# Optimization experiments

Hardware: AMD Instinct MI355X
Metric: run time of the kernel (lower is better)

Reference implementation:

```python
import jax, jax.numpy as jnp
import numpy as np

B, K, LQ, LR, H = 32, 8, 128, 256, 512  # H = hidden_dim*2
L = LQ + K * LR


def setup_inputs() -> dict:
    key = jax.random.key(0)
    ks = jax.random.split(key, 10)
    w = 0.02
    return {
        "h_q": jax.random.normal(ks[0], (B, LQ, H), jnp.float32),
        "q_mask": jnp.ones((B, LQ), jnp.float32),
        "h_r": jax.random.normal(ks[1], (B, K, LR, H), jnp.float32),
        "r_mask": jnp.ones((B, K, LR), jnp.float32),
        "s_t": jax.random.normal(ks[2], (B, H), jnp.float32),
        "qr_cov": jnp.zeros((B, L), jnp.float32),
        # Linear weights stored torch-style [out, in]
        "U_w": jax.random.normal(ks[3], (H, H), jnp.float32) * w,
        "Wc_w": jax.random.normal(ks[4], (H, 1), jnp.float32) * w,
        "Ws_w": jax.random.normal(ks[5], (H, H), jnp.float32) * w,
        "Wqr_w": jax.random.normal(ks[6], (H, H), jnp.float32) * w,
        "Wqr_b": jax.random.normal(ks[7], (H,), jnp.float32) * w,
        "Vr_w": jax.random.normal(ks[8], (1, H), jnp.float32) * w,
    }


def reference(h_q, q_mask, h_r, r_mask, s_t, qr_cov,
              U_w, Wc_w, Ws_w, Wqr_w, Wqr_b, Vr_w):
    b, l_q, h = h_q.shape
    _, k, l_r, _ = h_r.shape

    _h_q = jnp.broadcast_to(h_q[:, None], (b, k, l_q, h)).reshape(b * k, l_q, h)
    _h_r = h_r.reshape(b * k, l_r, h)
    _q_mask = jnp.broadcast_to(q_mask[:, None], (b, k, l_q)).reshape(b * k, l_q)
    _r_mask = r_mask.reshape(b * k, l_r)

    # bilinear co-attention scores: tanh((hq @ U^T) @ hr^T)  [b*k, l_q, l_r]
    hqU = jnp.einsum('bqi,oi->bqo', _h_q, U_w)
    U = jnp.tanh(jnp.einsum('bqo,bro->bqr', hqU, _h_r))

    alpha_q = jax.nn.softmax(jnp.max(U, axis=2), axis=-1)  # [b*k, l_q]
    alpha_r = jax.nn.softmax(jnp.max(U, axis=1), axis=-1)  # [b*k, l_r]

    pai_q = ((alpha_q * _q_mask)[..., None] * _h_q).reshape(b, k, l_q, h).mean(axis=1)
    pai_r = ((alpha_r * _r_mask)[..., None] * _h_r).reshape(b, k * l_r, h)
    qr = jnp.concatenate([pai_q, pai_r], axis=1)  # [b, L, h]

    dec_fea = (jnp.einsum('bi,oi->bo', s_t, Ws_w)[:, None, :]
               + jnp.einsum('bli,oi->blo', qr, Wqr_w) + Wqr_b
               + qr_cov[:, :, None] * Wc_w[:, 0])  # coverage feature

    logits = jnp.einsum('blo,o->bl', jnp.tanh(dec_fea), Vr_w[0])  # [b, L]
    mask = jnp.concatenate([q_mask, r_mask.reshape(b, k * l_r)], axis=1)
    a = jax.nn.softmax(logits, axis=1) * mask
    a = a / jnp.sum(a, axis=1, keepdims=True)

    c_t = jnp.einsum('bl,blh->bh', a, qr)
    new_cov = qr_cov + a
    return (c_t, a, new_cov)
```

## Files before the change

### kernel.cpp

```cpp
#include <hip/hip_runtime.h>
#include <stdint.h>

#define B  32
#define KK 8
#define LQ 128
#define LR 256
#define H  512
#define LL 2176
#define STRIDE 40

typedef short s16x8 __attribute__((ext_vector_type(8)));
typedef float f32x4 __attribute__((ext_vector_type(4)));

__device__ __forceinline__ unsigned short f2bf(float f) {
    unsigned int u = __float_as_uint(f);
    unsigned int r = (u + 0x7FFFu + ((u >> 16) & 1u)) >> 16;
    return (unsigned short)r;
}
__device__ __forceinline__ float bf2f(unsigned short h) {
    return __uint_as_float(((unsigned int)h) << 16);
}

__global__ __launch_bounds__(128) void k0_convert(
    const float* __restrict__ h_q, const float* __restrict__ h_r,
    const float* __restrict__ U_w, const float* __restrict__ Wqr_w,
    unsigned short* __restrict__ Xb, unsigned short* __restrict__ Uwb,
    unsigned short* __restrict__ Wqrb) {
    int blk = blockIdx.x;
    const float* src; unsigned short* dst;
    if (blk < B * LL) {
        int b = blk / LL, l = blk % LL;
        src = (l < LQ) ? (h_q + (size_t)(b * LQ + l) * H)
                       : (h_r + (size_t)(b * (KK * LR) + (l - LQ)) * H);
        dst = Xb + (size_t)blk * H;
    } else if (blk < B * LL + H) {
        int i = blk - B * LL;
        src = U_w + (size_t)i * H; dst = Uwb + (size_t)i * H;
    } else {
        int i = blk - B * LL - H;
        src = Wqr_w + (size_t)i * H; dst = Wqrb + (size_t)i * H;
    }
    int t = threadIdx.x;
    float4 v = *(const float4*)(src + t * 4);
    ushort4 o;
    o.x = f2bf(v.x); o.y = f2bf(v.y); o.z = f2bf(v.z); o.w = f2bf(v.w);
    *(ushort4*)(dst + t * 4) = o;
}

__global__ __launch_bounds__(256) void k1_gemm_hqU(
    const unsigned short* __restrict__ Xb, const unsigned short* __restrict__ Uwb,
    unsigned short* __restrict__ hqU) {
    __shared__ __align__(16) unsigned short As[64 * STRIDE];
    __shared__ __align__(16) unsigned short Bs[64 * STRIDE];
    int tid = threadIdx.x;
    int wave = tid >> 6, lane = tid & 63;
    int quad = lane >> 4, l16 = lane & 15;
    int wr = wave >> 1, wc = wave & 1;
    int m0 = blockIdx.x * 64, n0 = blockIdx.y * 64;

    f32x4 acc[2][2] = {};
    int srow = tid >> 2, sk8 = tid & 3;
    int am = m0 + srow;
    size_t arow = (size_t)(am >> 7) * LL + (am & 127);
    for (int k0 = 0; k0 < H; k0 += 32) {
        *(uint4*)&As[srow * STRIDE + sk8 * 8] =
            *(const uint4*)(Xb + arow * H + k0 + sk8 * 8);
        *(uint4*)&Bs[srow * STRIDE + sk8 * 8] =
            *(const uint4*)(Uwb + (size_t)(n0 + srow) * H + k0 + sk8 * 8);
        __syncthreads();
        s16x8 af[2], bfr[2];
#pragma unroll
        for (int mi = 0; mi < 2; ++mi)
            af[mi] = *(const s16x8*)&As[(wr * 32 + mi * 16 + l16) * STRIDE + quad * 8];
#pragma unroll
        for (int ni = 0; ni < 2; ++ni)
            bfr[ni] = *(const s16x8*)&Bs[(wc * 32 + ni * 16 + l16) * STRIDE + quad * 8];
#pragma unroll
        for (int mi = 0; mi < 2; ++mi)
#pragma unroll
            for (int ni = 0; ni < 2; ++ni)
                acc[mi][ni] = __builtin_amdgcn_mfma_f32_16x16x32_bf16(
                    af[mi], bfr[ni], acc[mi][ni], 0, 0, 0);
        __syncthreads();
    }
#pragma unroll
    for (int mi = 0; mi < 2; ++mi)
#pragma unroll
        for (int ni = 0; ni < 2; ++ni)
#pragma unroll
            for (int i = 0; i < 4; ++i) {
                int row = m0 + wr * 32 + mi * 16 + quad * 4 + i;
                int col = n0 + wc * 32 + ni * 16 + l16;
                hqU[(size_t)row * H + col] = f2bf(acc[mi][ni][i]);
            }
}

__global__ __launch_bounds__(256) void k2_scores(
    const unsigned short* __restrict__ hqU, const unsigned short* __restrict__ Xb,
    float* __restrict__ maxq_part, float* __restrict__ maxr_part) {
    __shared__ __align__(16) unsigned short As[64 * STRIDE];
    __shared__ __align__(16) unsigned short Bs[128 * STRIDE];
    __shared__ float redA[64 * 2];
    __shared__ float redB[128 * 2];
    int idx = blockIdx.x;
    int rt = idx & 1, qt = (idx >> 1) & 1, k = (idx >> 2) & 7, b = idx >> 5;
    int tid = threadIdx.x;
    int wave = tid >> 6, lane = tid & 63;
    int quad = lane >> 4, l16 = lane & 15;
    int wr = wave >> 1, wc = wave & 1;

    size_t aBase = (size_t)(b * LQ + qt * 64) * H;
    size_t bBase = (size_t)(b * LL + LQ + k * LR + rt * 128) * H;

    f32x4 acc[2][4] = {};
    int srow = tid >> 2, sk8 = tid & 3;
    for (int k0 = 0; k0 < H; k0 += 32) {
        *(uint4*)&As[srow * STRIDE + sk8 * 8] =
            *(const uint4*)(hqU + aBase + (size_t)srow * H + k0 + sk8 * 8);
        for (int c = tid; c < 512; c += 256) {
            int br = c >> 2, bk8 = c & 3;
            *(uint4*)&Bs[br * STRIDE + bk8 * 8] =
                *(const uint4*)(Xb + bBase + (size_t)br * H + k0 + bk8 * 8);
        }
        __syncthreads();
        s16x8 af[2], bfr[4];
#pragma unroll
        for (int mi = 0; mi < 2; ++mi)
            af[mi] = *(const s16x8*)&As[(wr * 32 + mi * 16 + l16) * STRIDE + quad * 8];
#pragma unroll
        for (int ni = 0; ni < 4; ++ni)
            bfr[ni] = *(const s16x8*)&Bs[(wc * 64 + ni * 16 + l16) * STRIDE + quad * 8];
#pragma unroll
        for (int mi = 0; mi < 2; ++mi)
#pragma unroll
            for (int ni = 0; ni < 4; ++ni)
                acc[mi][ni] = __builtin_amdgcn_mfma_f32_16x16x32_bf16(
                    af[mi], bfr[ni], acc[mi][ni], 0, 0, 0);
        __syncthreads();
    }
#pragma unroll
    for (int mi = 0; mi < 2; ++mi)
#pragma unroll
        for (int i = 0; i < 4; ++i) {
            float v = acc[mi][0][i];
            v = fmaxf(v, acc[mi][1][i]);
            v = fmaxf(v, acc[mi][2][i]);
            v = fmaxf(v, acc[mi][3][i]);
            for (int s = 1; s < 16; s <<= 1) v = fmaxf(v, __shfl_xor(v, s));
            if (l16 == 0) redA[(wr * 32 + mi * 16 + quad * 4 + i) * 2 + wc] = v;
        }
#pragma unroll
    for (int ni = 0; ni < 4; ++ni) {
        float v = acc[0][ni][0];
#pragma unroll
        for (int mi = 0; mi < 2; ++mi)
#pragma unroll
            for (int i = 0; i < 4; ++i) v = fmaxf(v, acc[mi][ni][i]);
        for (int s = 16; s < 64; s <<= 1) v = fmaxf(v, __shfl_xor(v, s));
        if (quad == 0) redB[(wc * 64 + ni * 16 + l16) * 2 + wr] = v;
    }
    __syncthreads();
    size_t base = (size_t)(b * KK + k);
    if (tid < 64) {
        float v = fmaxf(redA[tid * 2 + 0], redA[tid * 2 + 1]);
        maxq_part[(base * 2 + rt) * 128 + qt * 64 + tid] = v;
    }
    if (tid < 128) {
        float v = fmaxf(redB[tid * 2 + 0], redB[tid * 2 + 1]);
        maxr_part[(base * 2 + qt) * 256 + rt * 128 + tid] = v;
    }
}

__global__ __launch_bounds__(256) void k3a_alphas(
    const float* __restrict__ maxq_part, const float* __restrict__ maxr_part,
    const float* __restrict__ r_mask, float* __restrict__ alpha_q,
    float* __restrict__ wbuf) {
    int b = blockIdx.x >> 3, k = blockIdx.x & 7;
    int t = threadIdx.x;
    __shared__ float red[256];
    size_t base = (size_t)(b * KK + k);
    float vq = -1e30f;
    if (t < 128)
        vq = tanhf(fmaxf(maxq_part[(base * 2 + 0) * 128 + t],
                         maxq_part[(base * 2 + 1) * 128 + t]));
    red[t] = vq; __syncthreads();
    for (int s = 128; s > 0; s >>= 1) { if (t < s) red[t] = fmaxf(red[t], red[t + s]); __syncthreads(); }
    float mxq = red[0]; __syncthreads();
    float eq = (t < 128) ? expf(vq - mxq) : 0.f;
    red[t] = eq; __syncthreads();
    for (int s = 128; s > 0; s >>= 1) { if (t < s) red[t] += red[t + s]; __syncthreads(); }
    float invq = 1.f / red[0]; __syncthreads();
    if (t < 128) alpha_q[base * 128 + t] = eq * invq;
    float vr = tanhf(fmaxf(maxr_part[(base * 2 + 0) * 256 + t],
                           maxr_part[(base * 2 + 1) * 256 + t]));
    red[t] = vr; __syncthreads();
    for (int s = 128; s > 0; s >>= 1) { if (t < s) red[t] = fmaxf(red[t], red[t + s]); __syncthreads(); }
    float mxr = red[0]; __syncthreads();
    float er = expf(vr - mxr);
    red[t] = er; __syncthreads();
    for (int s = 128; s > 0; s >>= 1) { if (t < s) red[t] += red[t + s]; __syncthreads(); }
    float invr = 1.f / red[0];
    wbuf[b * LL + LQ + k * LR + t] = r_mask[base * LR + t] * er * invr;
}

__global__ __launch_bounds__(256) void k3b_wq_sws(
    const float* __restrict__ alpha_q, const float* __restrict__ q_mask,
    const float* __restrict__ s_t, const float* __restrict__ Ws_w,
    float* __restrict__ wbuf, float* __restrict__ logits,
    float* __restrict__ sWs, float* __restrict__ out_ct) {
    int b = blockIdx.x, t = threadIdx.x;
    for (int l = t; l < LL; l += 256) logits[b * LL + l] = 0.f;
    if (t < 128) {
        float s = 0.f;
#pragma unroll
        for (int k = 0; k < KK; ++k) s += alpha_q[(size_t)(b * KK + k) * 128 + t];
        wbuf[b * LL + t] = q_mask[b * LQ + t] * s * 0.125f;
    }
    out_ct[b * H + t] = 0.f;
    out_ct[b * H + 256 + t] = 0.f;
    __shared__ __align__(16) float sl[H];
    for (int i = t; i < H; i += 256) sl[i] = s_t[b * H + i];
    __syncthreads();
    const float4* sl4 = (const float4*)sl;
    for (int o = t; o < H; o += 256) {
        const float4* wr4 = (const float4*)(Ws_w + (size_t)o * H);
        float a = 0.f;
        for (int i = 0; i < H / 4; ++i) {
            float4 x = sl4[i], y = wr4[i];
            a += x.x * y.x + x.y * y.y + x.z * y.z + x.w * y.w;
        }
        sWs[b * H + o] = a;
    }
}

__global__ __launch_bounds__(256) void k4_gemm_logits(
    const unsigned short* __restrict__ Xb, const unsigned short* __restrict__ Wqrb,
    const float* __restrict__ sWs, const float* __restrict__ Wqr_b,
    const float* __restrict__ Wc_w, const float* __restrict__ Vr_w,
    const float* __restrict__ wbuf, const float* __restrict__ qr_cov,
    float* __restrict__ logits) {
    __shared__ __align__(16) unsigned short As[128 * STRIDE];
    __shared__ __align__(16) unsigned short Bs[128 * STRIDE];
    __shared__ float wrow[128], covrow[128], sWsl[128], biasl[128], wcl[128], vrl[128];
    int tid = threadIdx.x;
    int wave = tid >> 6, lane = tid & 63;
    int quad = lane >> 4, l16 = lane & 15;
    int wr = wave >> 1, wc = wave & 1;
    size_t m0 = (size_t)blockIdx.x * 128;
    int n0 = blockIdx.y * 128;
    int b = (int)(m0 / LL);
    int l0 = (int)(m0 % LL);

    f32x4 acc[4][4] = {};
    for (int k0 = 0; k0 < H; k0 += 32) {
        for (int c = tid; c < 512; c += 256) {
            int r = c >> 2, k8 = c & 3;
            *(uint4*)&As[r * STRIDE + k8 * 8] =
                *(const uint4*)(Xb + (m0 + r) * H + k0 + k8 * 8);
            *(uint4*)&Bs[r * STRIDE + k8 * 8] =
                *(const uint4*)(Wqrb + (size_t)(n0 + r) * H + k0 + k8 * 8);
        }
        __syncthreads();
        s16x8 af[4], bfr[4];
#pragma unroll
        for (int mi = 0; mi < 4; ++mi)
            af[mi] = *(const s16x8*)&As[(wr * 64 + mi * 16 + l16) * STRIDE + quad * 8];
#pragma unroll
        for (int ni = 0; ni < 4; ++ni)
            bfr[ni] = *(const s16x8*)&Bs[(wc * 64 + ni * 16 + l16) * STRIDE + quad * 8];
#pragma unroll
        for (int mi = 0; mi < 4; ++mi)
#pragma unroll
            for (int ni = 0; ni < 4; ++ni)
                acc[mi][ni] = __builtin_amdgcn_mfma_f32_16x16x32_bf16(
                    af[mi], bfr[ni], acc[mi][ni], 0, 0, 0);
        __syncthreads();
    }
    if (tid < 128) {
        wrow[tid]   = wbuf[b * LL + l0 + tid];
        covrow[tid] = qr_cov[b * LL + l0 + tid];
        sWsl[tid]   = sWs[b * H + n0 + tid];
        biasl[tid]  = Wqr_b[n0 + tid];
        wcl[tid]    = Wc_w[n0 + tid];
        vrl[tid]    = Vr_w[n0 + tid];
    }
    __syncthreads();
#pragma unroll
    for (int mi = 0; mi < 4; ++mi)
#pragma unroll
        for (int i = 0; i < 4; ++i) {
            int rl = wr * 64 + mi * 16 + quad * 4 + i;
            float wv = wrow[rl], cv = covrow[rl];
            float lsum = 0.f;
#pragma unroll
            for (int ni = 0; ni < 4; ++ni) {
                int ol = wc * 64 + ni * 16 + l16;
                float dec = sWsl[ol] + wv * acc[mi][ni][i] + biasl[ol] + cv * wcl[ol];
                lsum += vrl[ol] * tanhf(dec);
            }
            for (int s = 1; s < 16; s <<= 1) lsum += __shfl_xor(lsum, s);
            if (l16 == 0) atomicAdd(&logits[b * LL + l0 + rl], lsum);
        }
}

__global__ __launch_bounds__(256) void k5a_softmax(
    const float* __restrict__ logits, const float* __restrict__ q_mask,
    const float* __restrict__ r_mask, const float* __restrict__ qr_cov,
    const float* __restrict__ wbuf, float* __restrict__ out,
    float* __restrict__ coef) {
    int b = blockIdx.x, t = threadIdx.x;
    __shared__ float red[256];
    float mx = -1e30f;
    for (int l = t; l < LL; l += 256) mx = fmaxf(mx, logits[b * LL + l]);
    red[t] = mx; __syncthreads();
    for (int s = 128; s > 0; s >>= 1) { if (t < s) red[t] = fmaxf(red[t], red[t + s]); __syncthreads(); }
    mx = red[0]; __syncthreads();
    float sum = 0.f;
    for (int l = t; l < LL; l += 256) {
        float e = expf(logits[b * LL + l] - mx);
        float m = (l < LQ) ? q_mask[b * LQ + l] : r_mask[b * (KK * LR) + l - LQ];
        sum += e * m;
    }
    red[t] = sum; __syncthreads();
    for (int s = 128; s > 0; s >>= 1) { if (t < s) red[t] += red[t + s]; __syncthreads(); }
    float inv = 1.f / red[0];
    float* aout = out + B * H + (size_t)b * LL;
    float* cov  = out + B * H + (size_t)B * LL + (size_t)b * LL;
    for (int l = t; l < LL; l += 256) {
        float e = expf(logits[b * LL + l] - mx);
        float m = (l < LQ) ? q_mask[b * LQ + l] : r_mask[b * (KK * LR) + l - LQ];
        float a = e * m * inv;
        aout[l] = a;
        cov[l] = qr_cov[b * LL + l] + a;
        coef[b * LL + l] = a * wbuf[b * LL + l];
    }
}

__global__ __launch_bounds__(256) void k5b_ct(
    const unsigned short* __restrict__ Xb, const float* __restrict__ coef,
    float* __restrict__ out) {
    int b = blockIdx.x / 17, chunk = blockIdx.x % 17;
    int t = threadIdx.x;
    int l0 = chunk * 128;
    __shared__ float cl[128];
    if (t < 128) cl[t] = coef[b * LL + l0 + t];
    __syncthreads();
    float a0 = 0.f, a1 = 0.f;
    const unsigned short* xp = Xb + ((size_t)b * LL + l0) * H;
    for (int l = 0; l < 128; ++l) {
        float c = cl[l];
        a0 += c * bf2f(xp[(size_t)l * H + t]);
        a1 += c * bf2f(xp[(size_t)l * H + t + 256]);
    }
    atomicAdd(&out[b * H + t], a0);
    atomicAdd(&out[b * H + t + 256], a1);
}

extern "C" void kernel_launch(void* const* d_in, const int* in_sizes, int n_in,
                              void* d_out, int out_size, void* d_ws, size_t ws_size,
                              hipStream_t stream) {
    (void)in_sizes; (void)n_in; (void)out_size; (void)ws_size;
    const float* h_q    = (const float*)d_in[0];
    const float* q_mask = (const float*)d_in[1];
    const float* h_r    = (const float*)d_in[2];
    const float* r_mask = (const float*)d_in[3];
    const float* s_t    = (const float*)d_in[4];
    const float* qr_cov = (const float*)d_in[5];
    const float* U_w    = (const float*)d_in[6];
    const float* Wc_w   = (const float*)d_in[7];
    const float* Ws_w   = (const float*)d_in[8];
    const float* Wqr_w  = (const float*)d_in[9];
    const float* Wqr_b  = (const float*)d_in[10];
    const float* Vr_w   = (const float*)d_in[11];
    float* out = (float*)d_out;

    char* p = (char*)d_ws;
    unsigned short* Xb   = (unsigned short*)p; p += (size_t)B * LL * H * 2;
    unsigned short* Uwb  = (unsigned short*)p; p += (size_t)H * H * 2;
    unsigned short* Wqrb = (unsigned short*)p; p += (size_t)H * H * 2;
    unsigned short* hqU  = (unsigned short*)p; p += (size_t)B * LQ * H * 2;
    float* sWs       = (float*)p; p += (size_t)B * H * 4;
    float* maxq_part = (float*)p; p += (size_t)B * KK * 2 * 128 * 4;
    float* maxr_part = (float*)p; p += (size_t)B * KK * 2 * 256 * 4;
    float* alpha_q   = (float*)p; p += (size_t)B * KK * 128 * 4;
    float* wbuf      = (float*)p; p += (size_t)B * LL * 4;
    float* logits    = (float*)p; p += (size_t)B * LL * 4;
    float* coef      = (float*)p; p += (size_t)B * LL * 4;

    k0_convert<<<B * LL + 2 * H, 128, 0, stream>>>(h_q, h_r, U_w, Wqr_w, Xb, Uwb, Wqrb);
    k1_gemm_hqU<<<dim3((B * LQ) / 64, H / 64), 256, 0, stream>>>(Xb, Uwb, hqU);
    k2_scores<<<B * KK * 4, 256, 0, stream>>>(hqU, Xb, maxq_part, maxr_part);
    k3a_alphas<<<B * KK, 256, 0, stream>>>(maxq_part, maxr_part, r_mask, alpha_q, wbuf);
    k3b_wq_sws<<<B, 256, 0, stream>>>(alpha_q, q_mask, s_t, Ws_w, wbuf, logits, sWs, out);
    k4_gemm_logits<<<dim3((B * LL) / 128, H / 128), 256, 0, stream>>>(
        Xb, Wqrb, sWs, Wqr_b, Wc_w, Vr_w, wbuf, qr_cov, logits);
    k5a_softmax<<<B, 256, 0, stream>>>(logits, q_mask, r_mask, qr_cov, wbuf, out, coef);
    k5b_ct<<<B * (LL / 128), 256, 0, stream>>>(Xb, coef, out);
}
```

Before: 405.0 us.

## Use direct global-to-LDS loads with swizzle, parallelize sWs, vectorize c_t

```diff
diff --git a/kernel.cpp b/kernel.cpp
--- a/kernel.cpp
+++ b/kernel.cpp
@@ -20,13 +20,29 @@
 __device__ __forceinline__ float bf2f(unsigned short h) {
     return __uint_as_float(((unsigned int)h) << 16);
 }
-
+__device__ __forceinline__ void gload16(const unsigned short* g, unsigned short* l) {
+    __builtin_amdgcn_global_load_lds(
+        (const __attribute__((address_space(1))) void*)g,
+        (__attribute__((address_space(3))) void*)l, 16, 0, 0);
+}
+
+#define NCONV (B * LL + 2 * H)
+#define NZERO 168
 __global__ __launch_bounds__(128) void k0_convert(
     const float* __restrict__ h_q, const float* __restrict__ h_r,
     const float* __restrict__ U_w, const float* __restrict__ Wqr_w,
     unsigned short* __restrict__ Xb, unsigned short* __restrict__ Uwb,
-    unsigned short* __restrict__ Wqrb) {
+    unsigned short* __restrict__ Wqrb, float* __restrict__ logits,
+    float* __restrict__ out) {
     int blk = blockIdx.x;
+    int t = threadIdx.x;
+    if (blk >= NCONV) {
+        int base = (blk - NCONV) * 512 + t * 4;
+        float4 z = {0.f, 0.f, 0.f, 0.f};
+        if (base < B * LL) *(float4*)(logits + base) = z;
+        else *(float4*)(out + base - B * LL) = z;
+        return;
+    }
     const float* src; unsigned short* dst;
     if (blk < B * LL) {
         int b = blk / LL, l = blk % LL;
@@ -40,7 +56,6 @@
         int i = blk - B * LL - H;
         src = Wqr_w + (size_t)i * H; dst = Wqrb + (size_t)i * H;
     }
-    int t = threadIdx.x;
     float4 v = *(const float4*)(src + t * 4);
     ushort4 o;
     o.x = f2bf(v.x); o.y = f2bf(v.y); o.z = f2bf(v.z); o.w = f2bf(v.w);
@@ -98,8 +113,8 @@
 __global__ __launch_bounds__(256) void k2_scores(
     const unsigned short* __restrict__ hqU, const unsigned short* __restrict__ Xb,
     float* __restrict__ maxq_part, float* __restrict__ maxr_part) {
-    __shared__ __align__(16) unsigned short As[64 * STRIDE];
-    __shared__ __align__(16) unsigned short Bs[128 * STRIDE];
+    __shared__ __align__(16) unsigned short As[64 * 64];
+    __shared__ __align__(16) unsigned short Bs[128 * 64];
     __shared__ float redA[64 * 2];
     __shared__ float redB[128 * 2];
     int idx = blockIdx.x;
@@ -109,33 +124,55 @@
     int quad = lane >> 4, l16 = lane & 15;
     int wr = wave >> 1, wc = wave & 1;
 
-    size_t aBase = (size_t)(b * LQ + qt * 64) * H;
-    size_t bBase = (size_t)(b * LL + LQ + k * LR + rt * 128) * H;
+    const unsigned short* Ab = hqU + (size_t)(b * LQ + qt * 64) * H;
+    const unsigned short* Bb = Xb + (size_t)(b * LL + LQ + k * LR + rt * 128) * H;
+
+    const unsigned short* ag[2]; unsigned short* la[2];
+    const unsigned short* bg[4]; unsigned short* lb[4];
+#pragma unroll
+    for (int i = 0; i < 2; ++i) {
+        int g = (wave * 2 + i) * 64 + lane;
+        int r = g >> 3, c = g & 7, cs = c ^ (r & 7);
+        ag[i] = Ab + (size_t)r * H + cs * 8;
+        la[i] = As + (wave * 2 + i) * 512;
+    }
+#pragma unroll
+    for (int i = 0; i < 4; ++i) {
+        int g = (wave * 4 + i) * 64 + lane;
+        int r = g >> 3, c = g & 7, cs = c ^ (r & 7);
+        bg[i] = Bb + (size_t)r * H + cs * 8;
+        lb[i] = Bs + (wave * 4 + i) * 512;
+    }
 
     f32x4 acc[2][4] = {};
-    int srow = tid >> 2, sk8 = tid & 3;
-    for (int k0 = 0; k0 < H; k0 += 32) {
-        *(uint4*)&As[srow * STRIDE + sk8 * 8] =
-            *(const uint4*)(hqU + aBase + (size_t)srow * H + k0 + sk8 * 8);
-        for (int c = tid; c < 512; c += 256) {
-            int br = c >> 2, bk8 = c & 3;
-            *(uint4*)&Bs[br * STRIDE + bk8 * 8] =
-                *(const uint4*)(Xb + bBase + (size_t)br * H + k0 + bk8 * 8);
+    for (int k0 = 0; k0 < H; k0 += 64) {
+#pragma unroll
+        for (int i = 0; i < 2; ++i) gload16(ag[i] + k0, la[i]);
+#pragma unroll
+        for (int i = 0; i < 4; ++i) gload16(bg[i] + k0, lb[i]);
+        __syncthreads();
+#pragma unroll
+        for (int kh = 0; kh < 2; ++kh) {
+            s16x8 af[2], bfr[4];
+#pragma unroll
+            for (int mi = 0; mi < 2; ++mi) {
+                int row = wr * 32 + mi * 16 + l16;
+                int ch = (kh * 4 + quad) ^ (row & 7);
+                af[mi] = *(const s16x8*)&As[(row * 8 + ch) * 8];
+            }
+#pragma unroll
+            for (int ni = 0; ni < 4; ++ni) {
+                int row = wc * 64 + ni * 16 + l16;
+                int ch = (kh * 4 + quad) ^ (row & 7);
+                bfr[ni] = *(const s16x8*)&Bs[(row * 8 + ch) * 8];
+            }
+#pragma unroll
+            for (int mi = 0; mi < 2; ++mi)
+#pragma unroll
+                for (int ni = 0; ni < 4; ++ni)
+                    acc[mi][ni] = __builtin_amdgcn_mfma_f32_16x16x32_bf16(
+                        af[mi], bfr[ni], acc[mi][ni], 0, 0, 0);
         }
-        __syncthreads();
-        s16x8 af[2], bfr[4];
-#pragma unroll
-        for (int mi = 0; mi < 2; ++mi)
-            af[mi] = *(const s16x8*)&As[(wr * 32 + mi * 16 + l16) * STRIDE + quad * 8];
-#pragma unroll
-        for (int ni = 0; ni < 4; ++ni)
-            bfr[ni] = *(const s16x8*)&Bs[(wc * 64 + ni * 16 + l16) * STRIDE + quad * 8];
-#pragma unroll
-        for (int mi = 0; mi < 2; ++mi)
-#pragma unroll
-            for (int ni = 0; ni < 4; ++ni)
-                acc[mi][ni] = __builtin_amdgcn_mfma_f32_16x16x32_bf16(
-                    af[mi], bfr[ni], acc[mi][ni], 0, 0, 0);
         __syncthreads();
     }
 #pragma unroll
@@ -203,34 +240,33 @@
     wbuf[b * LL + LQ + k * LR + t] = r_mask[base * LR + t] * er * invr;
 }
 
-__global__ __launch_bounds__(256) void k3b_wq_sws(
+__global__ __launch_bounds__(256) void k3b_sws(
     const float* __restrict__ alpha_q, const float* __restrict__ q_mask,
     const float* __restrict__ s_t, const float* __restrict__ Ws_w,
-    float* __restrict__ wbuf, float* __restrict__ logits,
-    float* __restrict__ sWs, float* __restrict__ out_ct) {
-    int b = blockIdx.x, t = threadIdx.x;
-    for (int l = t; l < LL; l += 256) logits[b * LL + l] = 0.f;
-    if (t < 128) {
-        float s = 0.f;
-#pragma unroll
-        for (int k = 0; k < KK; ++k) s += alpha_q[(size_t)(b * KK + k) * 128 + t];
-        wbuf[b * LL + t] = q_mask[b * LQ + t] * s * 0.125f;
-    }
-    out_ct[b * H + t] = 0.f;
-    out_ct[b * H + 256 + t] = 0.f;
+    float* __restrict__ wbuf, float* __restrict__ sWs) {
+    int b = blockIdx.x, oc = blockIdx.y;
+    int t = threadIdx.x;
     __shared__ __align__(16) float sl[H];
     for (int i = t; i < H; i += 256) sl[i] = s_t[b * H + i];
     __syncthreads();
+    if (oc == 0 && t < 128) {
+        float s = 0.f;
+#pragma unroll
+        for (int k = 0; k < KK; ++k) s += alpha_q[(size_t)(b * KK + k) * 128 + t];
+        wbuf[b * LL + t] = q_mask[b * LQ + t] * s * 0.125f;
+    }
+    int o = oc * 64 + (t >> 2);
+    int part = t & 3;
     const float4* sl4 = (const float4*)sl;
-    for (int o = t; o < H; o += 256) {
-        const float4* wr4 = (const float4*)(Ws_w + (size_t)o * H);
-        float a = 0.f;
-        for (int i = 0; i < H / 4; ++i) {
-            float4 x = sl4[i], y = wr4[i];
-            a += x.x * y.x + x.y * y.y + x.z * y.z + x.w * y.w;
-        }
-        sWs[b * H + o] = a;
-    }
+    const float4* wr4 = (const float4*)(Ws_w + (size_t)o * H);
+    float a = 0.f;
+    for (int i = part * 32; i < part * 32 + 32; ++i) {
+        float4 x = sl4[i], y = wr4[i];
+        a += x.x * y.x + x.y * y.y + x.z * y.z + x.w * y.w;
+    }
+    a += __shfl_xor(a, 1);
+    a += __shfl_xor(a, 2);
+    if (part == 0) sWs[b * H + o] = a;
 }
 
 __global__ __launch_bounds__(256) void k4_gemm_logits(
@@ -239,8 +275,8 @@
     const float* __restrict__ Wc_w, const float* __restrict__ Vr_w,
     const float* __restrict__ wbuf, const float* __restrict__ qr_cov,
     float* __restrict__ logits) {
-    __shared__ __align__(16) unsigned short As[128 * STRIDE];
-    __shared__ __align__(16) unsigned short Bs[128 * STRIDE];
+    __shared__ __align__(16) unsigned short As[128 * 64];
+    __shared__ __align__(16) unsigned short Bs[128 * 64];
     __shared__ float wrow[128], covrow[128], sWsl[128], biasl[128], wcl[128], vrl[128];
     int tid = threadIdx.x;
     int wave = tid >> 6, lane = tid & 63;
@@ -251,29 +287,47 @@
     int b = (int)(m0 / LL);
     int l0 = (int)(m0 % LL);
 
+    const unsigned short* ag[4]; unsigned short* la[4];
+    const unsigned short* bg[4]; unsigned short* lb[4];
+#pragma unroll
+    for (int i = 0; i < 4; ++i) {
+        int g = (wave * 4 + i) * 64 + lane;
+        int r = g >> 3, c = g & 7, cs = c ^ (r & 7);
+        ag[i] = Xb + (m0 + r) * H + cs * 8;
+        bg[i] = Wqrb + (size_t)(n0 + r) * H + cs * 8;
+        la[i] = As + (wave * 4 + i) * 512;
+        lb[i] = Bs + (wave * 4 + i) * 512;
+    }
+
     f32x4 acc[4][4] = {};
-    for (int k0 = 0; k0 < H; k0 += 32) {
-        for (int c = tid; c < 512; c += 256) {
-            int r = c >> 2, k8 = c & 3;
-            *(uint4*)&As[r * STRIDE + k8 * 8] =
-                *(const uint4*)(Xb + (m0 + r) * H + k0 + k8 * 8);
-            *(uint4*)&Bs[r * STRIDE + k8 * 8] =
-                *(const uint4*)(Wqrb + (size_t)(n0 + r) * H + k0 + k8 * 8);
+    for (int k0 = 0; k0 < H; k0 += 64) {
+#pragma unroll
+        for (int i = 0; i < 4; ++i) gload16(ag[i] + k0, la[i]);
+#pragma unroll
+        for (int i = 0; i < 4; ++i) gload16(bg[i] + k0, lb[i]);
+        __syncthreads();
+#pragma unroll
+        for (int kh = 0; kh < 2; ++kh) {
+            s16x8 af[4], bfr[4];
+#pragma unroll
+            for (int mi = 0; mi < 4; ++mi) {
+                int row = wr * 64 + mi * 16 + l16;
+                int ch = (kh * 4 + quad) ^ (row & 7);
+                af[mi] = *(const s16x8*)&As[(row * 8 + ch) * 8];
+            }
+#pragma unroll
+            for (int ni = 0; ni < 4; ++ni) {
+                int row = wc * 64 + ni * 16 + l16;
+                int ch = (kh * 4 + quad) ^ (row & 7);
+                bfr[ni] = *(const s16x8*)&Bs[(row * 8 + ch) * 8];
+            }
+#pragma unroll
+            for (int mi = 0; mi < 4; ++mi)
+#pragma unroll
+                for (int ni = 0; ni < 4; ++ni)
+                    acc[mi][ni] = __builtin_amdgcn_mfma_f32_16x16x32_bf16(
+                        af[mi], bfr[ni], acc[mi][ni], 0, 0, 0);
         }
-        __syncthreads();
-        s16x8 af[4], bfr[4];
-#pragma unroll
-        for (int mi = 0; mi < 4; ++mi)
-            af[mi] = *(const s16x8*)&As[(wr * 64 + mi * 16 + l16) * STRIDE + quad * 8];
-#pragma unroll
-        for (int ni = 0; ni < 4; ++ni)
-            bfr[ni] = *(const s16x8*)&Bs[(wc * 64 + ni * 16 + l16) * STRIDE + quad * 8];
-#pragma unroll
-        for (int mi = 0; mi < 4; ++mi)
-#pragma unroll
-            for (int ni = 0; ni < 4; ++ni)
-                acc[mi][ni] = __builtin_amdgcn_mfma_f32_16x16x32_bf16(
-                    af[mi], bfr[ni], acc[mi][ni], 0, 0, 0);
         __syncthreads();
     }
     if (tid < 128) {
@@ -345,15 +399,22 @@
     __shared__ float cl[128];
     if (t < 128) cl[t] = coef[b * LL + l0 + t];
     __syncthreads();
-    float a0 = 0.f, a1 = 0.f;
+    int rr = t >> 7;
+    int cc = (t & 127) * 4;
+    float a0 = 0.f, a1 = 0.f, a2 = 0.f, a3 = 0.f;
     const unsigned short* xp = Xb + ((size_t)b * LL + l0) * H;
-    for (int l = 0; l < 128; ++l) {
-        float c = cl[l];
-        a0 += c * bf2f(xp[(size_t)l * H + t]);
-        a1 += c * bf2f(xp[(size_t)l * H + t + 256]);
-    }
-    atomicAdd(&out[b * H + t], a0);
-    atomicAdd(&out[b * H + t + 256], a1);
+    for (int l = 0; l < 128; l += 2) {
+        float c = cl[l + rr];
+        ushort4 u = *(const ushort4*)(xp + (size_t)(l + rr) * H + cc);
+        a0 += c * bf2f(u.x);
+        a1 += c * bf2f(u.y);
+        a2 += c * bf2f(u.z);
+        a3 += c * bf2f(u.w);
+    }
+    atomicAdd(&out[b * H + cc + 0], a0);
+    atomicAdd(&out[b * H + cc + 1], a1);
+    atomicAdd(&out[b * H + cc + 2], a2);
+    atomicAdd(&out[b * H + cc + 3], a3);
 }
 
 extern "C" void kernel_launch(void* const* d_in, const int* in_sizes, int n_in,
@@ -387,11 +448,12 @@
     float* logits    = (float*)p; p += (size_t)B * LL * 4;
     float* coef      = (float*)p; p += (size_t)B * LL * 4;
 
-    k0_convert<<<B * LL + 2 * H, 128, 0, stream>>>(h_q, h_r, U_w, Wqr_w, Xb, Uwb, Wqrb);
+    k0_convert<<<NCONV + NZERO, 128, 0, stream>>>(h_q, h_r, U_w, Wqr_w, Xb, Uwb, Wqrb,
+                                                  logits, out);
     k1_gemm_hqU<<<dim3((B * LQ) / 64, H / 64), 256, 0, stream>>>(Xb, Uwb, hqU);
     k2_scores<<<B * KK * 4, 256, 0, stream>>>(hqU, Xb, maxq_part, maxr_part);
     k3a_alphas<<<B * KK, 256, 0, stream>>>(maxq_part, maxr_part, r_mask, alpha_q, wbuf);
-    k3b_wq_sws<<<B, 256, 0, stream>>>(alpha_q, q_mask, s_t, Ws_w, wbuf, logits, sWs, out);
+    k3b_sws<<<dim3(B, 8), 256, 0, stream>>>(alpha_q, q_mask, s_t, Ws_w, wbuf, sWs);
     k4_gemm_logits<<<dim3((B * LL) / 128, H / 128), 256, 0, stream>>>(
         Xb, Wqrb, sWs, Wqr_b, Wc_w, Vr_w, wbuf, qr_cov, logits);
     k5a_softmax<<<B, 256, 0, stream>>>(logits, q_mask, r_mask, qr_cov, wbuf, out, coef);
```

After: 388.6 us. 1.04x faster.
